# Performance work log

Hardware: AMD Instinct MI355X
Metric: run time of the kernel (lower is better)

## Reference

```python
import jax, jax.numpy as jnp
import numpy as np

N = 50000   # nodes
E = 800000  # edges (avg degree 16)
D = 128     # feature dim (input = hidden = output)
EPS = 1e-6


def setup_inputs() -> dict:
    key = jax.random.key(0)
    ks = jax.random.split(key, 8)
    xav = np.sqrt(6.0 / (D + D)).astype(np.float32)  # xavier_uniform bound for [D,D]
    inp = {
        "x": jax.random.normal(ks[0], (N, D), dtype=jnp.float32),
        "edge_index": jax.random.randint(ks[1], (2, E), 0, N, dtype=jnp.int64),
    }
    for i in range(3):
        inp[f"W{i+1}"] = jax.random.uniform(ks[2 + i], (D, D), dtype=jnp.float32, minval=-xav, maxval=xav)
        inp[f"b{i+1}"] = jnp.zeros((D,), dtype=jnp.float32)
        inp[f"g{i+1}"] = jnp.ones((D,), dtype=jnp.float32)   # RMSNorm gain
    return inp


def _rmsnorm(x, g):
    # x: [N, D]
    return x * jax.lax.rsqrt(jnp.mean(x * x, axis=-1, keepdims=True) + EPS) * g


def _gcn_layer(x, src, dst, edge_norm, W, b):
    # x: [N, D_in] -> [N, D_out]; sparse gather-scatter over edges (incl. self-loops)
    h = x @ W                                   # [N, D_out]
    msg = h[src] * edge_norm[:, None]           # gather + scale, [E+N, D_out]
    agg = jax.ops.segment_sum(msg, dst, num_segments=N)  # scatter-add, [N, D_out]
    return agg + b


def reference(x, edge_index, W1, b1, g1, W2, b2, g2, W3, b3, g3):
    # GCNConv default: add self-loops, symmetric D^{-1/2}(A+I)D^{-1/2} normalization
    loop = jnp.arange(N, dtype=edge_index.dtype)
    src = jnp.concatenate([edge_index[0], loop])  # [E+N]
    dst = jnp.concatenate([edge_index[1], loop])  # [E+N]
    deg = jax.ops.segment_sum(jnp.ones_like(dst, dtype=x.dtype), dst, num_segments=N)
    dinv = jnp.where(deg > 0, jax.lax.rsqrt(jnp.maximum(deg, 1.0)), 0.0)
    edge_norm = dinv[src] * dinv[dst]             # [E+N]

    for W, b, g in ((W1, b1, g1), (W2, b2, g2), (W3, b3, g3)):
        h = _rmsnorm(x, g)                         # pre-norm
        x = jax.nn.relu(_gcn_layer(h, src, dst, edge_norm, W, b))
    return x
```

## Files before the change

kernel.cpp:

```cpp
#include <hip/hip_runtime.h>
#include <cstdint>
#include <cstddef>

#define NN 50000
#define EE 800000
#define DD 128
#define NBLK 196
#define RS 132


__device__ __forceinline__ void fma4(float4& a, float s, const float4& v) {
    a.x = fmaf(s, v.x, a.x);
    a.y = fmaf(s, v.y, a.y);
    a.z = fmaf(s, v.z, a.z);
    a.w = fmaf(s, v.w, a.w);
}

__device__ __forceinline__ unsigned int f2bf(float f) {
    unsigned int u = __float_as_uint(f);
    u += 0x7fffu + ((u >> 16) & 1u);
    return u >> 16;
}
__device__ __forceinline__ float bflo(unsigned int u) { return __uint_as_float(u << 16); }
__device__ __forceinline__ float bfhi(unsigned int u) { return __uint_as_float(u & 0xffff0000u); }

__device__ __forceinline__ int ld_idx(const int* __restrict__ p, long long i, int mode64) {
    return mode64 ? p[2 * i] : p[(size_t)i];
}

__global__ void probe_kernel(const int* __restrict__ ei, int* __restrict__ flag) {
    int t = threadIdx.x;
    int v = ei[2 * t + 1];
    unsigned long long b = __ballot(v != 0);
    if (t == 0) *flag = (b == 0ull) ? 1 : 0;
}

__global__ void count_kernel(const int* __restrict__ ei, const int* __restrict__ flag,
                             int* __restrict__ deg, int* __restrict__ rank) {
    int e = blockIdx.x * 256 + threadIdx.x;
    if (e >= EE) return;
    int m = *flag;
    int d = ld_idx(ei, (long long)EE + e, m);
    rank[e] = atomicAdd(&deg[d], 1);
}

__global__ __launch_bounds__(256) void partial_kernel(const int* __restrict__ deg,
                                                      int* __restrict__ bsum) {
    int idx = blockIdx.x * 256 + threadIdx.x;
    int v = (idx < NN) ? deg[idx] : 0;
    for (int off = 1; off < 64; off <<= 1) v += __shfl_xor(v, off);
    __shared__ int ws[4];
    if ((threadIdx.x & 63) == 0) ws[threadIdx.x >> 6] = v;
    __syncthreads();
    if (threadIdx.x == 0) bsum[blockIdx.x] = ws[0] + ws[1] + ws[2] + ws[3];
}

__global__ __launch_bounds__(256) void bscan_kernel(const int* __restrict__ bsum,
                                                    int* __restrict__ boff) {
    __shared__ int sh[256];
    int t = threadIdx.x;
    sh[t] = (t < NBLK) ? bsum[t] : 0;
    __syncthreads();
    for (int off = 1; off < 256; off <<= 1) {
        int u = (t >= off) ? sh[t - off] : 0;
        __syncthreads();
        sh[t] += u;
        __syncthreads();
    }
    if (t <= NBLK) boff[t] = (t == 0) ? 0 : sh[t - 1];
}

__global__ __launch_bounds__(256) void scatter_scan_kernel(
        const int* __restrict__ deg, const int* __restrict__ boff,
        int* __restrict__ row_ptr, float* __restrict__ dinv) {
    __shared__ int sh[256];
    int t = threadIdx.x;
    int idx = blockIdx.x * 256 + t;
    int v = (idx < NN) ? deg[idx] : 0;
    sh[t] = v;
    __syncthreads();
    for (int off = 1; off < 256; off <<= 1) {
        int u = (t >= off) ? sh[t - off] : 0;
        __syncthreads();
        sh[t] += u;
        __syncthreads();
    }
    if (idx < NN) {
        row_ptr[idx] = boff[blockIdx.x] + sh[t] - v;
        dinv[idx] = rsqrtf((float)(v + 1));
    }
    if (idx == 0) row_ptr[NN] = boff[NBLK];
}

__global__ void fill_kernel(const int* __restrict__ ei, const int* __restrict__ flag,
                            const int* __restrict__ row_ptr, const int* __restrict__ rank,
                            const float* __restrict__ dinv, uint2* __restrict__ csr) {
    int e = blockIdx.x * 256 + threadIdx.x;
    if (e >= EE) return;
    int m = *flag;
    int sv = ld_idx(ei, (long long)e, m);
    int dv = ld_idx(ei, (long long)EE + e, m);
    int pos = row_ptr[dv] + rank[e];
    csr[pos] = make_uint2((unsigned)sv, __float_as_uint(dinv[sv]));
}

__global__ __launch_bounds__(256) void rmsnorm_gemm_kernel(
        const float* __restrict__ X, const float* __restrict__ W,
        const float* __restrict__ g, unsigned int* __restrict__ H) {
    __shared__ float xn[64 * RS];
    int t = threadIdx.x;
    int row0 = blockIdx.x * 64;

    int r = t >> 2, part = t & 3;
    int row = row0 + r;
    float4 v[8];
    float ss = 0.f;
    if (row < NN) {
        const float4* xr = (const float4*)(X + (size_t)row * DD) + part * 8;
        #pragma unroll
        for (int i = 0; i < 8; i++) {
            v[i] = xr[i];
            ss += v[i].x * v[i].x + v[i].y * v[i].y + v[i].z * v[i].z + v[i].w * v[i].w;
        }
    } else {
        #pragma unroll
        for (int i = 0; i < 8; i++) v[i] = make_float4(0.f, 0.f, 0.f, 0.f);
    }
    ss += __shfl_xor(ss, 1);
    ss += __shfl_xor(ss, 2);
    float sc = rsqrtf(ss * (1.0f / DD) + 1e-6f);

    const float4* g4 = (const float4*)g + part * 8;
    float4* xrow = (float4*)(&xn[r * RS]) + part * 8;
    #pragma unroll
    for (int i = 0; i < 8; i++) {
        float4 gq = g4[i], q;
        q.x = v[i].x * sc * gq.x;
        q.y = v[i].y * sc * gq.y;
        q.z = v[i].z * sc * gq.z;
        q.w = v[i].w * sc * gq.w;
        xrow[i] = q;
    }
    __syncthreads();

    int tc = t & 31, tr = t >> 5;
    int r0 = tr * 8;
    const float4* W4 = (const float4*)W;
    float4 acc[8];
    #pragma unroll
    for (int i = 0; i < 8; i++) acc[i] = make_float4(0.f, 0.f, 0.f, 0.f);
    #pragma unroll 2
    for (int k = 0; k < DD; k += 4) {
        float4 w0 = W4[(k + 0) * 32 + tc];
        float4 w1 = W4[(k + 1) * 32 + tc];
        float4 w2 = W4[(k + 2) * 32 + tc];
        float4 w3 = W4[(k + 3) * 32 + tc];
        #pragma unroll
        for (int i = 0; i < 8; i++) {
            float4 xv = *(const float4*)&xn[(r0 + i) * RS + k];
            fma4(acc[i], xv.x, w0);
            fma4(acc[i], xv.y, w1);
            fma4(acc[i], xv.z, w2);
            fma4(acc[i], xv.w, w3);
        }
    }
    #pragma unroll
    for (int i = 0; i < 8; i++) {
        int rb = row0 + r0 + i;
        if (rb < NN) {
            uint2 o;
            o.x = f2bf(acc[i].x) | (f2bf(acc[i].y) << 16);
            o.y = f2bf(acc[i].z) | (f2bf(acc[i].w) << 16);
            ((uint2*)(H + (size_t)rb * 64))[tc] = o;
        }
    }
}

__global__ __launch_bounds__(256) void aggregate_kernel(
        const unsigned int* __restrict__ Hm, const float* __restrict__ dinv,
        const int* __restrict__ row_ptr, const uint2* __restrict__ csr,
        const float* __restrict__ b, float* __restrict__ out) {
    __shared__ uint2 sEdge[4][64];
    int wv = threadIdx.x >> 6;
    int lane = threadIdx.x & 63;
    int n = blockIdx.x * 4 + wv;
    int grp = lane >> 4;
    int tc = lane & 15;
    const uint4* H4 = (const uint4*)Hm;
    float dn = dinv[n];
    float acc[8];
    #pragma unroll
    for (int i = 0; i < 8; i++) acc[i] = 0.f;

    if (grp == 0) {
        uint4 q = H4[(size_t)n * 16 + tc];
        float w = dn * dn;
        const float4* b4 = (const float4*)b;
        float4 ba = b4[2 * tc], bb = b4[2 * tc + 1];
        acc[0] = fmaf(bflo(q.x), w, ba.x);
        acc[1] = fmaf(bfhi(q.x), w, ba.y);
        acc[2] = fmaf(bflo(q.y), w, ba.z);
        acc[3] = fmaf(bfhi(q.y), w, ba.w);
        acc[4] = fmaf(bflo(q.z), w, bb.x);
        acc[5] = fmaf(bfhi(q.z), w, bb.y);
        acc[6] = fmaf(bflo(q.w), w, bb.z);
        acc[7] = fmaf(bfhi(q.w), w, bb.w);
    }

    int start = row_ptr[n], end = row_ptr[n + 1];
    for (int base = start; base < end; base += 64) {
        int m = min(64, end - base);
        if (lane < m) sEdge[wv][lane] = csr[base + lane];
        for (int j = grp; j < m; j += 4) {
            uint2 p = sEdge[wv][j];
            int s = (int)p.x;
            float w = __uint_as_float(p.y) * dn;
            uint4 q = H4[(size_t)s * 16 + tc];
            acc[0] = fmaf(bflo(q.x), w, acc[0]);
            acc[1] = fmaf(bfhi(q.x), w, acc[1]);
            acc[2] = fmaf(bflo(q.y), w, acc[2]);
            acc[3] = fmaf(bfhi(q.y), w, acc[3]);
            acc[4] = fmaf(bflo(q.z), w, acc[4]);
            acc[5] = fmaf(bfhi(q.z), w, acc[5]);
            acc[6] = fmaf(bflo(q.w), w, acc[6]);
            acc[7] = fmaf(bfhi(q.w), w, acc[7]);
        }
    }

    #pragma unroll
    for (int i = 0; i < 8; i++) {
        acc[i] += __shfl_xor(acc[i], 16);
        acc[i] += __shfl_xor(acc[i], 32);
    }
    if (grp == 0) {
        float4 o0, o1;
        o0.x = fmaxf(acc[0], 0.f); o0.y = fmaxf(acc[1], 0.f);
        o0.z = fmaxf(acc[2], 0.f); o0.w = fmaxf(acc[3], 0.f);
        o1.x = fmaxf(acc[4], 0.f); o1.y = fmaxf(acc[5], 0.f);
        o1.z = fmaxf(acc[6], 0.f); o1.w = fmaxf(acc[7], 0.f);
        float4* orow = (float4*)(out + (size_t)n * DD + 8 * tc);
        orow[0] = o0;
        orow[1] = o1;
    }
}

extern "C" void kernel_launch(void* const* d_in, const int* in_sizes, int n_in,
                              void* d_out, int out_size, void* d_ws, size_t ws_size,
                              hipStream_t stream) {
    (void)in_sizes; (void)n_in; (void)out_size; (void)ws_size;
    const float* x  = (const float*)d_in[0];
    const int*   ei = (const int*)d_in[1];
    const float* W1 = (const float*)d_in[2];
    const float* b1 = (const float*)d_in[3];
    const float* g1 = (const float*)d_in[4];
    const float* W2 = (const float*)d_in[5];
    const float* b2 = (const float*)d_in[6];
    const float* g2 = (const float*)d_in[7];
    const float* W3 = (const float*)d_in[8];
    const float* b3 = (const float*)d_in[9];
    const float* g3 = (const float*)d_in[10];
    float* out = (float*)d_out;

    char* wsb = (char*)d_ws;
    int*   deg     = (int*)(wsb + 0);
    int*   bsum    = (int*)(wsb + 200000);
    int*   boff    = (int*)(wsb + 200832);
    int*   row_ptr = (int*)(wsb + 400000);
    int*   rank    = (int*)(wsb + 600064);
    float* dinv    = (float*)(wsb + 3800064);
    int*   flag    = (int*)(wsb + 4000064);
    unsigned int* Hb = (unsigned int*)(wsb + 4000256);
    uint2* csr     = (uint2*)(wsb + 16800256);

    hipMemsetAsync(deg, 0, 200000, stream);

    probe_kernel<<<1, 64, 0, stream>>>(ei, flag);
    count_kernel<<<(EE + 255) / 256, 256, 0, stream>>>(ei, flag, deg, rank);
    partial_kernel<<<NBLK, 256, 0, stream>>>(deg, bsum);
    bscan_kernel<<<1, 256, 0, stream>>>(bsum, boff);
    scatter_scan_kernel<<<NBLK, 256, 0, stream>>>(deg, boff, row_ptr, dinv);
    fill_kernel<<<(EE + 255) / 256, 256, 0, stream>>>(ei, flag, row_ptr, rank, dinv, csr);

    const int gemm_grid = (NN + 63) / 64;
    const int agg_grid  = NN / 4;

    rmsnorm_gemm_kernel<<<gemm_grid, 256, 0, stream>>>(x, W1, g1, Hb);
    aggregate_kernel<<<agg_grid, 256, 0, stream>>>(Hb, dinv, row_ptr, csr, b1, out);
    rmsnorm_gemm_kernel<<<gemm_grid, 256, 0, stream>>>(out, W2, g2, Hb);
    aggregate_kernel<<<agg_grid, 256, 0, stream>>>(Hb, dinv, row_ptr, csr, b2, out);
    rmsnorm_gemm_kernel<<<gemm_grid, 256, 0, stream>>>(out, W3, g3, Hb);
    aggregate_kernel<<<agg_grid, 256, 0, stream>>>(Hb, dinv, row_ptr, csr, b3, out);
}
```

Baseline: 357.6 us.

## Replace FP32 FMA GEMM with split-bf16 MFMA and unroll edge gather by two

Each layer's RMSNorm+GEMM now runs on MFMA matrix instructions. Activations and weights are split into bf16 hi/lo pairs, and three MFMAs per tile approximate fp32 accuracy. A small per-layer kernel converts and transposes W into the hi/lo bf16 layout, and LDS uses an XOR swizzle to avoid bank conflicts. The aggregate loop also handles two edges per iteration so more gathers are in flight. This adds extra launches and some precision loss compared with true fp32.

Result: slower. 375.8 us (+5.1%).

```diff
diff --git a/kernel.cpp b/kernel.cpp
--- a/kernel.cpp
+++ b/kernel.cpp
@@ -6,21 +6,17 @@
 #define EE 800000
 #define DD 128
 #define NBLK 196
-#define RS 132
-
-
-__device__ __forceinline__ void fma4(float4& a, float s, const float4& v) {
-    a.x = fmaf(s, v.x, a.x);
-    a.y = fmaf(s, v.y, a.y);
-    a.z = fmaf(s, v.z, a.z);
-    a.w = fmaf(s, v.w, a.w);
-}
+
+
+using bf16x8 = __attribute__((ext_vector_type(8))) short;
+using f32x4  = __attribute__((ext_vector_type(4))) float;
 
 __device__ __forceinline__ unsigned int f2bf(float f) {
     unsigned int u = __float_as_uint(f);
     u += 0x7fffu + ((u >> 16) & 1u);
     return u >> 16;
 }
+__device__ __forceinline__ float bf2f(unsigned int hi) { return __uint_as_float(hi << 16); }
 __device__ __forceinline__ float bflo(unsigned int u) { return __uint_as_float(u << 16); }
 __device__ __forceinline__ float bfhi(unsigned int u) { return __uint_as_float(u & 0xffff0000u); }
 
@@ -104,10 +100,22 @@
     csr[pos] = make_uint2((unsigned)sv, __float_as_uint(dinv[sv]));
 }
 
-__global__ __launch_bounds__(256) void rmsnorm_gemm_kernel(
-        const float* __restrict__ X, const float* __restrict__ W,
-        const float* __restrict__ g, unsigned int* __restrict__ H) {
-    __shared__ float xn[64 * RS];
+__global__ __launch_bounds__(256) void convw_kernel(const float* __restrict__ W,
+        unsigned short* __restrict__ WhT, unsigned short* __restrict__ WlT) {
+    int id = blockIdx.x * 256 + threadIdx.x;
+    int k = id >> 7, n = id & 127;
+    float w = W[id];
+    unsigned int hi = f2bf(w);
+    unsigned int lo = f2bf(w - bf2f(hi));
+    WhT[n * 128 + k] = (unsigned short)hi;
+    WlT[n * 128 + k] = (unsigned short)lo;
+}
+
+__global__ __launch_bounds__(256) void rmsnorm_mfma_kernel(
+        const float* __restrict__ X, const unsigned short* __restrict__ WhT,
+        const unsigned short* __restrict__ WlT, const float* __restrict__ g,
+        uint4* __restrict__ H) {
+    __shared__ uint4 smem[2048];
     int t = threadIdx.x;
     int row0 = blockIdx.x * 64;
 
@@ -131,48 +139,80 @@
     float sc = rsqrtf(ss * (1.0f / DD) + 1e-6f);
 
     const float4* g4 = (const float4*)g + part * 8;
-    float4* xrow = (float4*)(&xn[r * RS]) + part * 8;
-    #pragma unroll
-    for (int i = 0; i < 8; i++) {
-        float4 gq = g4[i], q;
-        q.x = v[i].x * sc * gq.x;
-        q.y = v[i].y * sc * gq.y;
-        q.z = v[i].z * sc * gq.z;
-        q.w = v[i].w * sc * gq.w;
-        xrow[i] = q;
-    }
-    __syncthreads();
-
-    int tc = t & 31, tr = t >> 5;
-    int r0 = tr * 8;
-    const float4* W4 = (const float4*)W;
-    float4 acc[8];
-    #pragma unroll
-    for (int i = 0; i < 8; i++) acc[i] = make_float4(0.f, 0.f, 0.f, 0.f);
-    #pragma unroll 2
-    for (int k = 0; k < DD; k += 4) {
-        float4 w0 = W4[(k + 0) * 32 + tc];
-        float4 w1 = W4[(k + 1) * 32 + tc];
-        float4 w2 = W4[(k + 2) * 32 + tc];
-        float4 w3 = W4[(k + 3) * 32 + tc];
-        #pragma unroll
-        for (int i = 0; i < 8; i++) {
-            float4 xv = *(const float4*)&xn[(r0 + i) * RS + k];
-            fma4(acc[i], xv.x, w0);
-            fma4(acc[i], xv.y, w1);
-            fma4(acc[i], xv.z, w2);
-            fma4(acc[i], xv.w, w3);
-        }
-    }
-    #pragma unroll
-    for (int i = 0; i < 8; i++) {
-        int rb = row0 + r0 + i;
-        if (rb < NN) {
-            uint2 o;
-            o.x = f2bf(acc[i].x) | (f2bf(acc[i].y) << 16);
-            o.y = f2bf(acc[i].z) | (f2bf(acc[i].w) << 16);
-            ((uint2*)(H + (size_t)rb * 64))[tc] = o;
-        }
+    #pragma unroll
+    for (int c = 0; c < 4; c++) {
+        float f[8];
+        #pragma unroll
+        for (int h = 0; h < 2; h++) {
+            float4 gq = g4[2 * c + h];
+            float4 xv = v[2 * c + h];
+            f[4 * h + 0] = xv.x * sc * gq.x;
+            f[4 * h + 1] = xv.y * sc * gq.y;
+            f[4 * h + 2] = xv.z * sc * gq.z;
+            f[4 * h + 3] = xv.w * sc * gq.w;
+        }
+        unsigned int hb[8], lb[8];
+        #pragma unroll
+        for (int j = 0; j < 8; j++) {
+            hb[j] = f2bf(f[j]);
+            lb[j] = f2bf(f[j] - bf2f(hb[j]));
+        }
+        uint4 hq, lq;
+        hq.x = hb[0] | (hb[1] << 16); hq.y = hb[2] | (hb[3] << 16);
+        hq.z = hb[4] | (hb[5] << 16); hq.w = hb[6] | (hb[7] << 16);
+        lq.x = lb[0] | (lb[1] << 16); lq.y = lb[2] | (lb[3] << 16);
+        lq.z = lb[4] | (lb[5] << 16); lq.w = lb[6] | (lb[7] << 16);
+        int idx = r * 16 + ((part * 4 + c) ^ (r & 7));
+        smem[idx] = hq;
+        smem[1024 + idx] = lq;
+    }
+    __syncthreads();
+
+    int w = t >> 6, lane = t & 63;
+    int kg = lane >> 4;
+    int arow = w * 16 + (lane & 15);
+    bf16x8 ah[4], al[4];
+    #pragma unroll
+    for (int kk = 0; kk < 4; kk++) {
+        int idx = arow * 16 + ((kk * 4 + kg) ^ (arow & 7));
+        ah[kk] = *(const bf16x8*)&smem[idx];
+        al[kk] = *(const bf16x8*)&smem[1024 + idx];
+    }
+    __syncthreads();
+
+    const bf16x8* whv = (const bf16x8*)WhT;
+    const bf16x8* wlv = (const bf16x8*)WlT;
+    f32x4 acc[8];
+    #pragma unroll
+    for (int nt = 0; nt < 8; nt++) acc[nt] = (f32x4){0.f, 0.f, 0.f, 0.f};
+    #pragma unroll
+    for (int nt = 0; nt < 8; nt++) {
+        int bi = (nt * 16 + (lane & 15)) * 16 + kg;
+        #pragma unroll
+        for (int kk = 0; kk < 4; kk++) {
+            bf16x8 bh = whv[bi + kk * 4];
+            bf16x8 bl = wlv[bi + kk * 4];
+            acc[nt] = __builtin_amdgcn_mfma_f32_16x16x32_bf16(ah[kk], bh, acc[nt], 0, 0, 0);
+            acc[nt] = __builtin_amdgcn_mfma_f32_16x16x32_bf16(al[kk], bh, acc[nt], 0, 0, 0);
+            acc[nt] = __builtin_amdgcn_mfma_f32_16x16x32_bf16(ah[kk], bl, acc[nt], 0, 0, 0);
+        }
+    }
+
+    unsigned short* hsm = (unsigned short*)smem;
+    #pragma unroll
+    for (int nt = 0; nt < 8; nt++) {
+        #pragma unroll
+        for (int q = 0; q < 4; q++) {
+            int rr = w * 16 + (lane >> 4) * 4 + q;
+            int cc = nt * 16 + (lane & 15);
+            hsm[rr * 128 + cc] = (unsigned short)f2bf(acc[nt][q]);
+        }
+    }
+    __syncthreads();
+    if (row < NN) {
+        #pragma unroll
+        for (int c = 0; c < 4; c++)
+            H[(size_t)row * 16 + part * 4 + c] = smem[r * 16 + part * 4 + c];
     }
 }
 
@@ -211,11 +251,35 @@
     for (int base = start; base < end; base += 64) {
         int m = min(64, end - base);
         if (lane < m) sEdge[wv][lane] = csr[base + lane];
-        for (int j = grp; j < m; j += 4) {
+        int j = grp;
+        for (; j + 4 < m; j += 8) {
+            uint2 p0 = sEdge[wv][j];
+            uint2 p1 = sEdge[wv][j + 4];
+            uint4 q0 = H4[(size_t)p0.x * 16 + tc];
+            uint4 q1 = H4[(size_t)p1.x * 16 + tc];
+            float w0 = __uint_as_float(p0.y) * dn;
+            float w1 = __uint_as_float(p1.y) * dn;
+            acc[0] = fmaf(bflo(q0.x), w0, acc[0]);
+            acc[1] = fmaf(bfhi(q0.x), w0, acc[1]);
+            acc[2] = fmaf(bflo(q0.y), w0, acc[2]);
+            acc[3] = fmaf(bfhi(q0.y), w0, acc[3]);
+            acc[4] = fmaf(bflo(q0.z), w0, acc[4]);
+            acc[5] = fmaf(bfhi(q0.z), w0, acc[5]);
+            acc[6] = fmaf(bflo(q0.w), w0, acc[6]);
+            acc[7] = fmaf(bfhi(q0.w), w0, acc[7]);
+            acc[0] = fmaf(bflo(q1.x), w1, acc[0]);
+            acc[1] = fmaf(bfhi(q1.x), w1, acc[1]);
+            acc[2] = fmaf(bflo(q1.y), w1, acc[2]);
+            acc[3] = fmaf(bfhi(q1.y), w1, acc[3]);
+            acc[4] = fmaf(bflo(q1.z), w1, acc[4]);
+            acc[5] = fmaf(bfhi(q1.z), w1, acc[5]);
+            acc[6] = fmaf(bflo(q1.w), w1, acc[6]);
+            acc[7] = fmaf(bfhi(q1.w), w1, acc[7]);
+        }
+        if (j < m) {
             uint2 p = sEdge[wv][j];
-            int s = (int)p.x;
+            uint4 q = H4[(size_t)p.x * 16 + tc];
             float w = __uint_as_float(p.y) * dn;
-            uint4 q = H4[(size_t)s * 16 + tc];
             acc[0] = fmaf(bflo(q.x), w, acc[0]);
             acc[1] = fmaf(bfhi(q.x), w, acc[1]);
             acc[2] = fmaf(bflo(q.y), w, acc[2]);
@@ -271,6 +335,8 @@
     int*   flag    = (int*)(wsb + 4000064);
     unsigned int* Hb = (unsigned int*)(wsb + 4000256);
     uint2* csr     = (uint2*)(wsb + 16800256);
+    unsigned short* WhT = (unsigned short*)(wsb + 23200256);
+    unsigned short* WlT = (unsigned short*)(wsb + 23233024);
 
     hipMemsetAsync(deg, 0, 200000, stream);
 
@@ -283,11 +349,17 @@
 
     const int gemm_grid = (NN + 63) / 64;
     const int agg_grid  = NN / 4;
-
-    rmsnorm_gemm_kernel<<<gemm_grid, 256, 0, stream>>>(x, W1, g1, Hb);
+    uint4* H4 = (uint4*)Hb;
+
+    convw_kernel<<<64, 256, 0, stream>>>(W1, WhT, WlT);
+    rmsnorm_mfma_kernel<<<gemm_grid, 256, 0, stream>>>(x, WhT, WlT, g1, H4);
     aggregate_kernel<<<agg_grid, 256, 0, stream>>>(Hb, dinv, row_ptr, csr, b1, out);
-    rmsnorm_gemm_kernel<<<gemm_grid, 256, 0, stream>>>(out, W2, g2, Hb);
+
+    convw_kernel<<<64, 256, 0, stream>>>(W2, WhT, WlT);
+    rmsnorm_mfma_kernel<<<gemm_grid, 256, 0, stream>>>(out, WhT, WlT, g2, H4);
     aggregate_kernel<<<agg_grid, 256, 0, stream>>>(Hb, dinv, row_ptr, csr, b2, out);
-    rmsnorm_gemm_kernel<<<gemm_grid, 256, 0, stream>>>(out, W3, g3, Hb);
+
+    convw_kernel<<<64, 256, 0, stream>>>(W3, WhT, WlT);
+    rmsnorm_mfma_kernel<<<gemm_grid, 256, 0, stream>>>(out, WhT, WlT, g3, H4);
     aggregate_kernel<<<agg_grid, 256, 0, stream>>>(Hb, dinv, row_ptr, csr, b3, out);
 }
```
